# Performance work log

Hardware: AMD Instinct MI355X
Metric: run time of the kernel (lower is better)

Reference implementation:

```python
import jax, jax.numpy as jnp
import numpy as np


def setup_inputs() -> dict:
    key = jax.random.key(0)
    B, H, W = 16, 1024, 1024
    x = jax.random.uniform(key, (B, H, W), dtype=jnp.float32)
    return {"x": x, "bit_depth": 1}


def reference(x, bit_depth):
    # --- reduce_color_depth: quantize via truncating int cast (torch .int()) ---
    scale = 255.0 / (2 ** bit_depth - 1)
    xq = jnp.trunc(x * scale) / scale

    # --- spatial_smoothing: 3x3 median filter with reflect padding ---
    B, H, W = xq.shape
    xp = jnp.pad(xq, ((0, 0), (1, 1), (1, 1)), mode="reflect")  # [B, H+2, W+2]
    # stack the 9 shifted views -> [B, H, W, 9] (same as unfold+view)
    patches = jnp.stack(
        [xp[:, i:i + H, j:j + W] for i in range(3) for j in range(3)], axis=-1
    )
    # odd window (9) -> median is the middle order statistic, matching torch.median
    return jnp.median(patches, axis=-1)
```

## Files before the change

kernel.cpp:

```cpp
#include <hip/hip_runtime.h>
#include <math.h>


constexpr int H = 1024;
constexpr int W = 1024;
constexpr int TY = 8;
constexpr int NROWS = TY + 2;
constexpr int LDSW = 1028;

#define S2(a, b) { float _mn = fminf(a, b); b = fmaxf(a, b); a = _mn; }

__device__ __forceinline__ void sort3(float& a, float& b, float& c) {
    S2(a, b); S2(b, c); S2(a, b);
}

__device__ __forceinline__ float merge9(float p0, float p1, float p2,
                                        float p3, float p4, float p5,
                                        float p6, float p7, float p8) {
    S2(p0, p3); S2(p5, p8); S2(p4, p7);
    S2(p3, p6); S2(p1, p4); S2(p2, p5);
    S2(p4, p7); S2(p4, p2); S2(p6, p4);
    S2(p4, p2);
    return p4;
}

__global__ __launch_bounds__(256) void fsq_kernel(const float* __restrict__ x,
                                                  const int* __restrict__ bdp,
                                                  float* __restrict__ out) {
    __shared__ float tile[NROWS * LDSW];

    const int t  = threadIdx.x;
    const int y0 = blockIdx.x * TY;
    const int b  = blockIdx.y;

    const float q     = (float)((1 << bdp[0]) - 1);
    const float scale = 255.0f / q;
    const float rinv  = q / 255.0f;

    const size_t base = (size_t)b * H * W;
    const float* __restrict__ xb = x + base;
    float* __restrict__ ob       = out + base;

    #pragma unroll
    for (int r = 0; r < NROWS; ++r) {
        int gy = y0 - 1 + r;
        gy = (gy < 0) ? 1 : ((gy >= H) ? 2 * H - 2 - gy : gy);
        const float4 v = *(const float4*)(xb + (size_t)gy * W + 4 * t);
        float4 qv;
        qv.x = truncf(v.x * scale) * rinv;
        qv.y = truncf(v.y * scale) * rinv;
        qv.z = truncf(v.z * scale) * rinv;
        qv.w = truncf(v.w * scale) * rinv;
        *(float4*)(&tile[r * LDSW + 4 * t]) = qv;
    }
    if (t < 2 * NROWS) {
        int r = t >> 1, side = t & 1;
        int gy = y0 - 1 + r;
        gy = (gy < 0) ? 1 : ((gy >= H) ? 2 * H - 2 - gy : gy);
        int gx = side ? 1 : 1022;
        tile[r * LDSW + 1024 + side] = truncf(xb[(size_t)gy * W + gx] * scale) * rinv;
    }
    __syncthreads();

    const int cL = (t == 0) ? 1025 : (4 * t - 1);
    const int cR = 4 * t + 4;

    float s0[4][3], s1[4][3], s2[4][3];
    float v[6];

    auto loadrow = [&](int r, float* vv) {
        const float* row = &tile[r * LDSW];
        float4 m = *(const float4*)(row + 4 * t);
        vv[0] = row[cL];
        vv[1] = m.x; vv[2] = m.y; vv[3] = m.z; vv[4] = m.w;
        vv[5] = row[cR];
    };

    loadrow(0, v);
    #pragma unroll
    for (int c = 0; c < 4; ++c) {
        s0[c][0] = v[c]; s0[c][1] = v[c + 1]; s0[c][2] = v[c + 2];
        sort3(s0[c][0], s0[c][1], s0[c][2]);
    }
    loadrow(1, v);
    #pragma unroll
    for (int c = 0; c < 4; ++c) {
        s1[c][0] = v[c]; s1[c][1] = v[c + 1]; s1[c][2] = v[c + 2];
        sort3(s1[c][0], s1[c][1], s1[c][2]);
    }

    #pragma unroll
    for (int r = 2; r < NROWS; ++r) {
        loadrow(r, v);
        #pragma unroll
        for (int c = 0; c < 4; ++c) {
            s2[c][0] = v[c]; s2[c][1] = v[c + 1]; s2[c][2] = v[c + 2];
            sort3(s2[c][0], s2[c][1], s2[c][2]);
        }
        float4 o;
        o.x = merge9(s0[0][0], s0[0][1], s0[0][2], s1[0][0], s1[0][1], s1[0][2], s2[0][0], s2[0][1], s2[0][2]);
        o.y = merge9(s0[1][0], s0[1][1], s0[1][2], s1[1][0], s1[1][1], s1[1][2], s2[1][0], s2[1][1], s2[1][2]);
        o.z = merge9(s0[2][0], s0[2][1], s0[2][2], s1[2][0], s1[2][1], s1[2][2], s2[2][0], s2[2][1], s2[2][2]);
        o.w = merge9(s0[3][0], s0[3][1], s0[3][2], s1[3][0], s1[3][1], s1[3][2], s2[3][0], s2[3][1], s2[3][2]);
        *(float4*)(ob + (size_t)(y0 + r - 2) * W + 4 * t) = o;

        #pragma unroll
        for (int c = 0; c < 4; ++c) {
            #pragma unroll
            for (int k = 0; k < 3; ++k) { s0[c][k] = s1[c][k]; s1[c][k] = s2[c][k]; }
        }
    }
}

extern "C" void kernel_launch(void* const* d_in, const int* in_sizes, int n_in,
                              void* d_out, int out_size, void* d_ws, size_t ws_size,
                              hipStream_t stream) {
    const float* x  = (const float*)d_in[0];
    const int*   bd = (const int*)d_in[1];
    float*       out = (float*)d_out;

    const int B = in_sizes[0] / (H * W);
    dim3 grid(H / TY, B);
    fsq_kernel<<<grid, 256, 0, stream>>>(x, bd, out);
}
```

Before: 116.0 us.

## Compute 3x3 median via column sorts with fmed3/min3/max3 primitives

Replaces the per-output row-sort plus merge network with a column-wise approach. Each 3-element column is sorted once with min3/med3/max3 and reused across four adjacent outputs, and each median is the med3 of max-of-lows, med-of-mids and min-of-highs. The hardware fmed3 instruction and fused min3/max3 patterns are meant to cut ALU instruction count substantially. The kernel is likely memory-bound at this size, so the compute savings may not show up in runtime.

```diff
diff --git a/kernel.cpp b/kernel.cpp
--- a/kernel.cpp
+++ b/kernel.cpp
@@ -8,21 +8,9 @@
 constexpr int NROWS = TY + 2;
 constexpr int LDSW = 1028;
 
-#define S2(a, b) { float _mn = fminf(a, b); b = fmaxf(a, b); a = _mn; }
-
-__device__ __forceinline__ void sort3(float& a, float& b, float& c) {
-    S2(a, b); S2(b, c); S2(a, b);
-}
-
-__device__ __forceinline__ float merge9(float p0, float p1, float p2,
-                                        float p3, float p4, float p5,
-                                        float p6, float p7, float p8) {
-    S2(p0, p3); S2(p5, p8); S2(p4, p7);
-    S2(p3, p6); S2(p1, p4); S2(p2, p5);
-    S2(p4, p7); S2(p4, p2); S2(p6, p4);
-    S2(p4, p2);
-    return p4;
-}
+__device__ __forceinline__ float min3f(float a, float b, float c) { return fminf(a, fminf(b, c)); }
+__device__ __forceinline__ float max3f(float a, float b, float c) { return fmaxf(a, fmaxf(b, c)); }
+__device__ __forceinline__ float med3f(float a, float b, float c) { return __builtin_amdgcn_fmed3f(a, b, c); }
 
 __global__ __launch_bounds__(256) void fsq_kernel(const float* __restrict__ x,
                                                   const int* __restrict__ bdp,
@@ -65,8 +53,7 @@
     const int cL = (t == 0) ? 1025 : (4 * t - 1);
     const int cR = 4 * t + 4;
 
-    float s0[4][3], s1[4][3], s2[4][3];
-    float v[6];
+    float r0[6], r1[6], r2[6];
 
     auto loadrow = [&](int r, float* vv) {
         const float* row = &tile[r * LDSW];
@@ -76,39 +63,30 @@
         vv[5] = row[cR];
     };
 
-    loadrow(0, v);
-    #pragma unroll
-    for (int c = 0; c < 4; ++c) {
-        s0[c][0] = v[c]; s0[c][1] = v[c + 1]; s0[c][2] = v[c + 2];
-        sort3(s0[c][0], s0[c][1], s0[c][2]);
-    }
-    loadrow(1, v);
-    #pragma unroll
-    for (int c = 0; c < 4; ++c) {
-        s1[c][0] = v[c]; s1[c][1] = v[c + 1]; s1[c][2] = v[c + 2];
-        sort3(s1[c][0], s1[c][1], s1[c][2]);
-    }
+    loadrow(0, r0);
+    loadrow(1, r1);
 
     #pragma unroll
     for (int r = 2; r < NROWS; ++r) {
-        loadrow(r, v);
+        loadrow(r, r2);
+
+        float lo[6], mi[6], hi[6];
         #pragma unroll
-        for (int c = 0; c < 4; ++c) {
-            s2[c][0] = v[c]; s2[c][1] = v[c + 1]; s2[c][2] = v[c + 2];
-            sort3(s2[c][0], s2[c][1], s2[c][2]);
+        for (int c = 0; c < 6; ++c) {
+            lo[c] = min3f(r0[c], r1[c], r2[c]);
+            mi[c] = med3f(r0[c], r1[c], r2[c]);
+            hi[c] = max3f(r0[c], r1[c], r2[c]);
         }
+
         float4 o;
-        o.x = merge9(s0[0][0], s0[0][1], s0[0][2], s1[0][0], s1[0][1], s1[0][2], s2[0][0], s2[0][1], s2[0][2]);
-        o.y = merge9(s0[1][0], s0[1][1], s0[1][2], s1[1][0], s1[1][1], s1[1][2], s2[1][0], s2[1][1], s2[1][2]);
-        o.z = merge9(s0[2][0], s0[2][1], s0[2][2], s1[2][0], s1[2][1], s1[2][2], s2[2][0], s2[2][1], s2[2][2]);
-        o.w = merge9(s0[3][0], s0[3][1], s0[3][2], s1[3][0], s1[3][1], s1[3][2], s2[3][0], s2[3][1], s2[3][2]);
+        o.x = med3f(max3f(lo[0], lo[1], lo[2]), med3f(mi[0], mi[1], mi[2]), min3f(hi[0], hi[1], hi[2]));
+        o.y = med3f(max3f(lo[1], lo[2], lo[3]), med3f(mi[1], mi[2], mi[3]), min3f(hi[1], hi[2], hi[3]));
+        o.z = med3f(max3f(lo[2], lo[3], lo[4]), med3f(mi[2], mi[3], mi[4]), min3f(hi[2], hi[3], hi[4]));
+        o.w = med3f(max3f(lo[3], lo[4], lo[5]), med3f(mi[3], mi[4], mi[5]), min3f(hi[3], hi[4], hi[5]));
         *(float4*)(ob + (size_t)(y0 + r - 2) * W + 4 * t) = o;
 
         #pragma unroll
-        for (int c = 0; c < 4; ++c) {
-            #pragma unroll
-            for (int k = 0; k < 3; ++k) { s0[c][k] = s1[c][k]; s1[c][k] = s2[c][k]; }
-        }
+        for (int c = 0; c < 6; ++c) { r0[c] = r1[c]; r1[c] = r2[c]; }
     }
 }
 
```

Result: no change. 114.8 us (-1.0%).
